# Optimization experiments

Measured on AMD Instinct MI355X. Metric: run time of the kernel, lower is better.

## Reference

```python
import jax, jax.numpy as jnp
import numpy as np

B, N, D = 4, 4096, 256

def setup_inputs() -> dict:
    key = jax.random.key(0)
    k1, = jax.random.split(key, 1)
    x = jax.random.normal(k1, (B, N, D), dtype=jnp.float32)
    attn_mask = jnp.ones((B, 1, N), dtype=jnp.int32)
    pad_mask = jnp.ones((B, 1, N), dtype=jnp.int32)
    return {"x": x, "attn_mask": attn_mask, "pad_mask": pad_mask, "dim_": D}

def reference(x, attn_mask, pad_mask, dim_):
    # adj is None -> scores = x @ x^T / sqrt(d)
    scale = jnp.sqrt(jnp.asarray(x.shape[-1], x.dtype))
    scores = jnp.einsum('bnd,bmd->bnm', x, x) / scale  # [B, N, N]
    # NOTE: original calls non-in-place masked_fill and discards the result,
    # so pad_mask / attn_mask have no effect on the output (faithful).
    prob = jax.nn.softmax(scores, axis=-1)
    # dropout is identity in inference mode
    return jnp.einsum('bnm,bmd->bnd', prob, x)
```

## Files before the change

### kernel.cpp

```cpp
#include <hip/hip_runtime.h>

typedef __attribute__((ext_vector_type(8))) short short8;
typedef __attribute__((ext_vector_type(4))) float f32x4;
typedef __attribute__((ext_vector_type(4))) unsigned int u32x4;

#define NTOK 4096
#define DIM  256
#define P_STRIDE 72
#define TILE_ELEMS 32768

__device__ __forceinline__ unsigned pack2bf(float a, float b) {
  unsigned ua = __builtin_bit_cast(unsigned, a) + 0x8000u;
  unsigned ub = __builtin_bit_cast(unsigned, b) + 0x8000u;
  return __builtin_amdgcn_perm(ub, ua, 0x07060302u);
}

__global__ __launch_bounds__(256, 4)
void prep_kernel(const float* __restrict__ X, unsigned short* __restrict__ Img) {
  __shared__ __align__(16) unsigned short rowbf[8 * 256];
  const int b    = blockIdx.x & 3;
  const int sub  = blockIdx.x >> 2;
  const int t    = sub >> 3;
  const int part = sub & 7;
  const int tid  = threadIdx.x;
  const float* src = X + ((size_t)b * NTOK + t * 64 + part * 8) * DIM;
  unsigned short* dst = Img + ((size_t)(b * 64 + t)) * TILE_ELEMS;
  {
    const int r = tid >> 5;
    const int c = tid & 31;
    const float* s = src + r * DIM + c * 8;
    f32x4 f0 = *(const f32x4*)s;
    f32x4 f1 = *(const f32x4*)(s + 4);
    union { unsigned u[4]; u32x4 v; } p;
    p.u[0] = pack2bf(f0[0], f0[1]);
    p.u[1] = pack2bf(f0[2], f0[3]);
    p.u[2] = pack2bf(f1[0], f1[1]);
    p.u[3] = pack2bf(f1[2], f1[3]);
    const int gr = part * 8 + r;
    *(u32x4*)(dst + gr * 256 + ((c ^ (gr & 7)) << 3)) = p.v;
    *(u32x4*)(&rowbf[r * 256 + c * 8]) = p.v;
  }
  __syncthreads();
  {
    const int d = tid;
    union { unsigned short s[8]; u32x4 v; } p;
    #pragma unroll
    for (int i = 0; i < 8; ++i) p.s[i] = rowbf[i * 256 + d];
    *(u32x4*)(dst + 16384 + part * 2048 + d * 8) = p.v;
  }
}

#define FA_STEP(T, VLD, VUS)                                                   \
  {                                                                            \
    const int t_ = (T);                                                        \
    __syncthreads();                                                           \
    const int buf_ = t_ & 1;                                                   \
    if (!isQK) {                                                               \
      if (t_ < 63) {                                                           \
        const char* g = gK + (size_t)(t_ + 1) * 65536;                         \
        unsigned short* l = &ksb[buf_ ^ 1][role * 4096];                       \
        _Pragma("unroll")                                                      \
        for (int i = 0; i < 8; ++i)                                            \
          __builtin_amdgcn_global_load_lds(                                    \
              (const __attribute__((address_space(1))) unsigned*)(g + i*1024), \
              (__attribute__((address_space(3))) unsigned*)(l + i*512),        \
              16, 0, 0);                                                       \
      }                                                                        \
      {                                                                        \
        const unsigned short* vt = vtg + (size_t)t_ * TILE_ELEMS;              \
        _Pragma("unroll")                                                      \
        for (int ks = 0; ks < 2; ++ks)                                         \
          _Pragma("unroll")                                                    \
          for (int dt = 0; dt < 4; ++dt)                                       \
            u[(VLD) + ks * 4 + dt] = __builtin_bit_cast(f32x4,                 \
                *(const short8*)(vt + (ks * 4 + quad) * 2048 + dt * 128));     \
      }                                                                        \
      if (t_ > 0) {                                                            \
        const unsigned short* prd = pb[buf_ ^ 1];                              \
        _Pragma("unroll")                                                      \
        for (int ks = 0; ks < 2; ++ks) {                                       \
          const int pos = (ks * 4 + quad) ^ ((ln >> 3) << 1);                  \
          _Pragma("unroll")                                                    \
          for (int s = 0; s < 4; ++s) {                                        \
            short8 ap = *(const short8*)(                                      \
                &prd[(s * 16 + ln) * P_STRIDE + (pos << 3)]);                  \
            _Pragma("unroll")                                                  \
            for (int dt = 0; dt < 4; ++dt)                                     \
              u[s * 4 + dt] = __builtin_amdgcn_mfma_f32_16x16x32_bf16(         \
                  ap, __builtin_bit_cast(short8, u[(VUS) + ks * 4 + dt]),      \
                  u[s * 4 + dt], 0, 0, 0);                                     \
          }                                                                    \
        }                                                                      \
      }                                                                        \
    } else {                                                                   \
      const unsigned short* krow = &ksb[buf_][(role * 16 + ln) * 256];         \
      f32x4 sf[4];                                                             \
      _Pragma("unroll")                                                        \
      for (int s = 0; s < 4; ++s) sf[s] = (f32x4)(0.0f);                       \
      _Pragma("unroll")                                                        \
      for (int ds = 0; ds < 8; ++ds) {                                         \
        short8 bk = *(const short8*)(krow + (((ds * 4 + quad) ^ swz) << 3));   \
        _Pragma("unroll")                                                      \
        for (int s = 0; s < 4; ++s)                                            \
          sf[s] = __builtin_amdgcn_mfma_f32_16x16x32_bf16(                     \
              __builtin_bit_cast(short8, u[s * 8 + ds]), bk, sf[s], 0, 0, 0);  \
      }                                                                        \
      unsigned pd[4][4];                                                       \
      _Pragma("unroll")                                                        \
      for (int s = 0; s < 4; ++s)                                              \
        _Pragma("unroll")                                                      \
        for (int j = 0; j < 4; ++j) {                                          \
          float p0 = __builtin_amdgcn_exp2f(sf[s][j] * c2);                    \
          lrow[s][j] += p0;                                                    \
          unsigned q0 = __builtin_bit_cast(unsigned, p0);                      \
          unsigned n0 = (unsigned)__builtin_amdgcn_mov_dpp((int)q0, 0xB1,      \
                                                           0xF, 0xF, true);   \
          pd[s][j] = pack2bf(p0, __builtin_bit_cast(float, n0));               \
        }                                                                      \
      if ((ln & 1) == 0) {                                                     \
        unsigned short* pw = pb[buf_];                                         \
        _Pragma("unroll")                                                      \
        for (int s = 0; s < 4; ++s)                                            \
          _Pragma("unroll")                                                    \
          for (int j = 0; j < 4; ++j)                                          \
            *(unsigned*)(&pw[(s * 16 + quad * 4 + j) * P_STRIDE +              \
                             pwPos + pwCol]) = pd[s][j];                       \
      }                                                                        \
    }                                                                          \
  }

__global__ __launch_bounds__(512, 1)
void fa_kernel(const unsigned short* __restrict__ Img, float* __restrict__ Out) {
  __shared__ __align__(16) unsigned short ksb[2][16384];
  __shared__ __align__(16) unsigned short pb[2][64 * P_STRIDE];
  __shared__ float lbuf[64][4];

  const int tid  = threadIdx.x;
  const int b    = blockIdx.x & 3;
  const int qblk = blockIdx.x >> 2;
  const int wave = tid >> 6;
  const int lane = tid & 63;
  const int ln   = lane & 15;
  const int quad = lane >> 4;
  const int swz  = ln & 7;
  const bool isQK = wave < 4;
  const int  role = wave & 3;

  const unsigned short* imgb  = Img + (size_t)b * 64 * TILE_ELEMS;
  const char*           imgbc = (const char*)imgb;

  const float c2 = 0.0901684400f;

  const int pwPos = ((role * 2 + (ln >> 3)) ^ ((quad >> 1) << 1)) << 3;
  const int pwCol = ln & 7;

  const char* gK = imgbc + (size_t)role * 8192 + (size_t)lane * 16;
  const unsigned short* vtg = imgb + 16384 + (size_t)(role * 64 + ln) * 8;

  float lrow[4][4] = {{0,0,0,0},{0,0,0,0},{0,0,0,0},{0,0,0,0}};

  f32x4 u[32];
  if (isQK) {
    #pragma unroll
    for (int s = 0; s < 4; ++s) {
      const unsigned short* qrow =
          imgb + (size_t)qblk * TILE_ELEMS + (s * 16 + ln) * 256;
      #pragma unroll
      for (int ds = 0; ds < 8; ++ds)
        u[s * 8 + ds] = __builtin_bit_cast(f32x4,
            *(const short8*)(qrow + (((ds * 4 + quad) ^ swz) << 3)));
    }
  } else {
    #pragma unroll
    for (int i = 0; i < 16; ++i) u[i] = (f32x4)(0.0f);
    #pragma unroll
    for (int i = 0; i < 8; ++i)
      __builtin_amdgcn_global_load_lds(
          (const __attribute__((address_space(1))) unsigned*)(gK + i * 1024),
          (__attribute__((address_space(3))) unsigned*)(&ksb[0][role * 4096 + i * 512]),
          16, 0, 0);
  }

  FA_STEP(0, 16, 24);
  #pragma unroll 1
  for (int tt = 1; tt < 63; tt += 2) {
    FA_STEP(tt, 24, 16);
    FA_STEP(tt + 1, 16, 24);
  }
  FA_STEP(63, 24, 16);

  __syncthreads();

  if (isQK) {
    #pragma unroll
    for (int off = 1; off < 16; off <<= 1)
      #pragma unroll
      for (int s = 0; s < 4; ++s)
        #pragma unroll
        for (int j = 0; j < 4; ++j)
          lrow[s][j] += __shfl_xor(lrow[s][j], off, 64);
    if (ln == 0) {
      #pragma unroll
      for (int s = 0; s < 4; ++s)
        #pragma unroll
        for (int j = 0; j < 4; ++j)
          lbuf[s * 16 + quad * 4 + j][role] = lrow[s][j];
    }
  } else {
    const unsigned short* prd = pb[1];
    #pragma unroll
    for (int ks = 0; ks < 2; ++ks) {
      const int pos = (ks * 4 + quad) ^ ((ln >> 3) << 1);
      #pragma unroll
      for (int s = 0; s < 4; ++s) {
        short8 ap = *(const short8*)(&prd[(s * 16 + ln) * P_STRIDE + (pos << 3)]);
        #pragma unroll
        for (int dt = 0; dt < 4; ++dt)
          u[s * 4 + dt] = __builtin_amdgcn_mfma_f32_16x16x32_bf16(
              ap, __builtin_bit_cast(short8, u[24 + ks * 4 + dt]),
              u[s * 4 + dt], 0, 0, 0);
      }
    }
  }
  __syncthreads();

  if (!isQK) {
    float* outB = Out + (size_t)(b * NTOK + qblk * 64) * DIM + role * 64;
    #pragma unroll
    for (int s = 0; s < 4; ++s) {
      #pragma unroll
      for (int j = 0; j < 4; ++j) {
        const int row = s * 16 + quad * 4 + j;
        f32x4 lv = *(const f32x4*)lbuf[row];
        const float rl = 1.0f / (lv[0] + lv[1] + lv[2] + lv[3]);
        #pragma unroll
        for (int dt = 0; dt < 4; ++dt)
          outB[(size_t)row * DIM + dt * 16 + ln] = u[s * 4 + dt][j] * rl;
      }
    }
  }
}

extern "C" void kernel_launch(void* const* d_in, const int* in_sizes, int n_in,
                              void* d_out, int out_size, void* d_ws, size_t ws_size,
                              hipStream_t stream) {
  const float* X = (const float*)d_in[0];
  float* Out = (float*)d_out;
  unsigned short* Img = (unsigned short*)d_ws;
  (void)in_sizes; (void)n_in; (void)out_size; (void)ws_size;
  hipLaunchKernelGGL(prep_kernel, dim3(2048), dim3(256), 0, stream, X, Img);
  hipLaunchKernelGGL(fa_kernel, dim3(256), dim3(512), 0, stream, Img, Out);
}
```

Before: 163.4 us.

## Load K tiles directly from global into registers instead of LDS staging

The PV waves no longer prefetch K tiles into a double-buffered shared-memory buffer via global_load_lds. The QK waves instead read their K rows straight from global memory into registers, which removes the K LDS buffer and the LDS read traffic. MFMA sections are wrapped in s_setprio raises, and the P write is restructured per s-slice. This drops the overlap of K prefetch with compute, so global load latency now sits on the QK critical path unless the L2 hides it.

```diff
diff --git a/kernel.cpp b/kernel.cpp
--- a/kernel.cpp
+++ b/kernel.cpp
@@ -53,19 +53,9 @@
 #define FA_STEP(T, VLD, VUS)                                                   \
   {                                                                            \
     const int t_ = (T);                                                        \
-    __syncthreads();                                                           \
+    __syncthreads();            \
     const int buf_ = t_ & 1;                                                   \
     if (!isQK) {                                                               \
-      if (t_ < 63) {                                                           \
-        const char* g = gK + (size_t)(t_ + 1) * 65536;                         \
-        unsigned short* l = &ksb[buf_ ^ 1][role * 4096];                       \
-        _Pragma("unroll")                                                      \
-        for (int i = 0; i < 8; ++i)                                            \
-          __builtin_amdgcn_global_load_lds(                                    \
-              (const __attribute__((address_space(1))) unsigned*)(g + i*1024), \
-              (__attribute__((address_space(3))) unsigned*)(l + i*512),        \
-              16, 0, 0);                                                       \
-      }                                                                        \
       {                                                                        \
         const unsigned short* vt = vtg + (size_t)t_ * TILE_ELEMS;              \
         _Pragma("unroll")                                                      \
@@ -77,6 +67,7 @@
       }                                                                        \
       if (t_ > 0) {                                                            \
         const unsigned short* prd = pb[buf_ ^ 1];                              \
+        __builtin_amdgcn_s_setprio(1);                                         \
         _Pragma("unroll")                                                      \
         for (int ks = 0; ks < 2; ++ks) {                                       \
           const int pos = (ks * 4 + quad) ^ ((ln >> 3) << 1);                  \
@@ -91,23 +82,32 @@
                   u[s * 4 + dt], 0, 0, 0);                                     \
           }                                                                    \
         }                                                                      \
+        __builtin_amdgcn_s_setprio(0);                                         \
       }                                                                        \
     } else {                                                                   \
-      const unsigned short* krow = &ksb[buf_][(role * 16 + ln) * 256];         \
+                    \
+      const unsigned short* kR =                                               \
+          imgb + (size_t)t_ * TILE_ELEMS + (role * 16 + ln) * 256;             \
+      short8 bk[8];                                                            \
+      _Pragma("unroll")                                                        \
+      for (int ds = 0; ds < 8; ++ds)                                           \
+        bk[ds] = *(const short8*)(kR + (((ds * 4 + quad) ^ swz) << 3));        \
       f32x4 sf[4];                                                             \
       _Pragma("unroll")                                                        \
       for (int s = 0; s < 4; ++s) sf[s] = (f32x4)(0.0f);                       \
-      _Pragma("unroll")                                                        \
-      for (int ds = 0; ds < 8; ++ds) {                                         \
-        short8 bk = *(const short8*)(krow + (((ds * 4 + quad) ^ swz) << 3));   \
+      __builtin_amdgcn_s_setprio(1);                                           \
+      _Pragma("unroll")                                                        \
+      for (int ds = 0; ds < 8; ++ds)                                           \
         _Pragma("unroll")                                                      \
         for (int s = 0; s < 4; ++s)                                            \
           sf[s] = __builtin_amdgcn_mfma_f32_16x16x32_bf16(                     \
-              __builtin_bit_cast(short8, u[s * 8 + ds]), bk, sf[s], 0, 0, 0);  \
-      }                                                                        \
-      unsigned pd[4][4];                                                       \
-      _Pragma("unroll")                                                        \
-      for (int s = 0; s < 4; ++s)                                              \
+              __builtin_bit_cast(short8, u[s * 8 + ds]), bk[ds], sf[s],        \
+              0, 0, 0);                                                        \
+      __builtin_amdgcn_s_setprio(0);                                           \
+      unsigned short* pw = pb[buf_];                                           \
+      _Pragma("unroll")                                                        \
+      for (int s = 0; s < 4; ++s) {                                            \
+        unsigned pd[4];                                                        \
         _Pragma("unroll")                                                      \
         for (int j = 0; j < 4; ++j) {                                          \
           float p0 = __builtin_amdgcn_exp2f(sf[s][j] * c2);                    \
@@ -115,23 +115,20 @@
           unsigned q0 = __builtin_bit_cast(unsigned, p0);                      \
           unsigned n0 = (unsigned)__builtin_amdgcn_mov_dpp((int)q0, 0xB1,      \
                                                            0xF, 0xF, true);   \
-          pd[s][j] = pack2bf(p0, __builtin_bit_cast(float, n0));               \
+          pd[j] = pack2bf(p0, __builtin_bit_cast(float, n0));                  \
         }                                                                      \
-      if ((ln & 1) == 0) {                                                     \
-        unsigned short* pw = pb[buf_];                                         \
-        _Pragma("unroll")                                                      \
-        for (int s = 0; s < 4; ++s)                                            \
+        if ((ln & 1) == 0) {                                                   \
           _Pragma("unroll")                                                    \
           for (int j = 0; j < 4; ++j)                                          \
             *(unsigned*)(&pw[(s * 16 + quad * 4 + j) * P_STRIDE +              \
-                             pwPos + pwCol]) = pd[s][j];                       \
+                             pwPos + pwCol]) = pd[j];                          \
+        }                                                                      \
       }                                                                        \
     }                                                                          \
   }
 
 __global__ __launch_bounds__(512, 1)
 void fa_kernel(const unsigned short* __restrict__ Img, float* __restrict__ Out) {
-  __shared__ __align__(16) unsigned short ksb[2][16384];
   __shared__ __align__(16) unsigned short pb[2][64 * P_STRIDE];
   __shared__ float lbuf[64][4];
 
@@ -146,15 +143,13 @@
   const bool isQK = wave < 4;
   const int  role = wave & 3;
 
-  const unsigned short* imgb  = Img + (size_t)b * 64 * TILE_ELEMS;
-  const char*           imgbc = (const char*)imgb;
+  const unsigned short* imgb = Img + (size_t)b * 64 * TILE_ELEMS;
 
   const float c2 = 0.0901684400f;
 
   const int pwPos = ((role * 2 + (ln >> 3)) ^ ((quad >> 1) << 1)) << 3;
   const int pwCol = ln & 7;
 
-  const char* gK = imgbc + (size_t)role * 8192 + (size_t)lane * 16;
   const unsigned short* vtg = imgb + 16384 + (size_t)(role * 64 + ln) * 8;
 
   float lrow[4][4] = {{0,0,0,0},{0,0,0,0},{0,0,0,0},{0,0,0,0}};
@@ -173,12 +168,6 @@
   } else {
     #pragma unroll
     for (int i = 0; i < 16; ++i) u[i] = (f32x4)(0.0f);
-    #pragma unroll
-    for (int i = 0; i < 8; ++i)
-      __builtin_amdgcn_global_load_lds(
-          (const __attribute__((address_space(1))) unsigned*)(gK + i * 1024),
-          (__attribute__((address_space(3))) unsigned*)(&ksb[0][role * 4096 + i * 512]),
-          16, 0, 0);
   }
 
   FA_STEP(0, 16, 24);
```

Measured after the change: 163.8 us. Within noise of the previous version (+0.2%).
